# Optimization experiments

Hardware: AMD Instinct MI355X
Metric: run time of the kernel (lower is better)

## Reference

```python
import jax, jax.numpy as jnp
import numpy as np

DECAY = 0.99
EPS = 1e-05
N, K, D = 32768, 8192, 64


def setup_inputs() -> dict:
    key = jax.random.key(0)
    k1, k2, k3 = jax.random.split(key, 3)
    return {
        "inputs": jax.random.normal(k1, (N, D), dtype=jnp.float32),
        "embedding_w": jax.random.normal(k2, (K, D), dtype=jnp.float32),
        "ema_w": jax.random.normal(k3, (K, D), dtype=jnp.float32),
        "ema_cluster_size": jnp.zeros((K,), dtype=jnp.float32),
    }


def reference(inputs, embedding_w, ema_w, ema_cluster_size):
    k = embedding_w.shape[0]
    # pairwise squared L2 distances: [N, K]
    distances = (
        jnp.sum(inputs ** 2, axis=1, keepdims=True)
        + jnp.sum(embedding_w ** 2, axis=1)
        - 2.0 * inputs @ embedding_w.T
    )
    encoding_indices = jnp.argmin(distances, axis=1)           # [N] int
    encodings = jax.nn.one_hot(encoding_indices, k, dtype=inputs.dtype)  # [N, K]
    codebook = embedding_w  # returned codebook is the PRE-update weight (as in torch source)

    # EMA updates (training branch), expressed functionally
    cluster_size = ema_cluster_size * DECAY + (1.0 - DECAY) * jnp.sum(encodings, axis=0)
    n = jnp.sum(cluster_size)
    cluster_size = (cluster_size + EPS) / (n + k * EPS) * n
    dw = encodings.T @ inputs                                   # [K, D]
    ema_w_new = ema_w * DECAY + (1.0 - DECAY) * dw
    embedding_new = ema_w_new / cluster_size[:, None]

    return (encodings, codebook, cluster_size, ema_w_new, embedding_new)
```

## Files before the change

kernel.cpp:

```cpp
#include <hip/hip_runtime.h>
#include <hip/hip_bf16.h>

#define N_PTS 32768
#define K_CLU 8192
#define D_DIM 64
#define DECAYF 0.99f
#define OMDF   0.01f
#define EPSF   1e-5f

typedef _Float16 v8h __attribute__((ext_vector_type(8)));
typedef float    v4f __attribute__((ext_vector_type(4)));

#define AS1 __attribute__((address_space(1)))
#define AS3 __attribute__((address_space(3)))

#define OFF_COUNTS 0
#define OFF_DW     (32768)
#define OFF_NSUM   (OFF_DW + 2097152)
#define OFF_EHI    (OFF_NSUM + 16)
#define OFF_ELO    (OFF_EHI + 1048576)
#define OFF_E2     (OFF_ELO + 1048576)

__global__ __launch_bounds__(256) void vq_prep(
    const float* __restrict__ emb, const float* __restrict__ ema_cs,
    _Float16* __restrict__ ehi, _Float16* __restrict__ elo,
    float* __restrict__ e2, float* __restrict__ nsum)
{
    const int wave = threadIdx.x >> 6;
    const int lane = threadIdx.x & 63;
    if (blockIdx.x < 2048) {
        const int row = blockIdx.x * 4 + wave;
        float v = emb[(size_t)row * D_DIM + lane];
        _Float16 h = (_Float16)v;
        _Float16 l = (_Float16)(v - (float)h);
        const int sw = (lane & 7) | ((((lane >> 3) ^ (row & 7)) & 7) << 3);
        ehi[(size_t)row * D_DIM + sw] = h;
        elo[(size_t)row * D_DIM + sw] = l;
        float s = v * v;
        #pragma unroll
        for (int m = 1; m < 64; m <<= 1) s += __shfl_xor(s, m, 64);
        if (lane == 0) e2[row] = s;
    } else {
        const int t = (blockIdx.x - 2048) * 256 + threadIdx.x;
        float v = ema_cs[t];
        #pragma unroll
        for (int m = 1; m < 64; m <<= 1) v += __shfl_xor(v, m, 64);
        if (lane == 0) atomicAdd(nsum, v);
    }
}

__global__ __launch_bounds__(256) void vq_fused(
    const float* __restrict__ x,
    const _Float16* __restrict__ ehi, const _Float16* __restrict__ elo,
    const float* __restrict__ e2,
    float* __restrict__ enc,
    unsigned int* __restrict__ counts,
    float* __restrict__ dw)
{
    __shared__ _Float16 sEhi[2][128 * 64];
    __shared__ _Float16 sElo[2][128 * 64];
    __shared__ float    sE2[2][128];

    const int bid  = blockIdx.x;
    const int tid  = threadIdx.x;
    const int wave = tid >> 6;
    const int lane = tid & 63;
    const int quad = lane >> 4;
    const int l15  = lane & 15;
    const int ptbase = bid * 64 + wave * 16;

    v8h xh[2], xl[2];
    {
        const int pt = ptbase + l15;
        const float* xp = x + (size_t)pt * D_DIM + quad * 8;
        #pragma unroll
        for (int c = 0; c < 2; ++c) {
            float4 a = *(const float4*)(xp + c * 32);
            float4 b = *(const float4*)(xp + c * 32 + 4);
            float vv[8] = {a.x, a.y, a.z, a.w, b.x, b.y, b.z, b.w};
            v8h hh, ll;
            #pragma unroll
            for (int j = 0; j < 8; ++j) {
                _Float16 h = (_Float16)vv[j];
                hh[j] = h;
                ll[j] = (_Float16)(vv[j] - (float)h);
            }
            xh[c] = hh; xl[c] = ll;
        }
    }

    float best[4]; int bidx4[4];
    #pragma unroll
    for (int i = 0; i < 4; ++i) { best[i] = 3.4e38f; bidx4[i] = 0; }

    v4f* enc4 = (v4f*)enc;
    const size_t zbase = (size_t)bid * 131072 + tid;
    const v4f zz = {0.f, 0.f, 0.f, 0.f};

    auto stage = [&](int b, int chunk) {
        const size_t gb = (size_t)chunk * 128 * 128;
        const char* gh = (const char*)ehi + gb;
        const char* gl = (const char*)elo + gb;
        char* lh = (char*)&sEhi[b][0];
        char* ll = (char*)&sElo[b][0];
        #pragma unroll
        for (int i = 0; i < 4; ++i) {
            const int off = wave * 4096 + i * 1024;
            __builtin_amdgcn_global_load_lds(
                (const AS1 void*)(gh + off + lane * 16), (AS3 void*)(lh + off), 16, 0, 0);
            __builtin_amdgcn_global_load_lds(
                (const AS1 void*)(gl + off + lane * 16), (AS3 void*)(ll + off), 16, 0, 0);
        }
        if (wave == 0) {
            const char* ge = (const char*)(e2 + (size_t)chunk * 128);
            char* le = (char*)&sE2[b][0];
            #pragma unroll
            for (int i = 0; i < 2; ++i) {
                __builtin_amdgcn_global_load_lds(
                    (const AS1 void*)(ge + i * 256 + lane * 4), (AS3 void*)(le + i * 256), 4, 0, 0);
            }
        }
    };

    stage(0, 0);
    asm volatile("s_waitcnt vmcnt(0)" ::: "memory");
    __builtin_amdgcn_s_barrier();
    __builtin_amdgcn_sched_barrier(0);

    for (int chunk = 0; chunk < 64; ++chunk) {
        const int cur = chunk & 1;
        if (chunk + 1 < 64) stage(cur ^ 1, chunk + 1);
        __builtin_amdgcn_sched_barrier(0);

        const int kbase = chunk * 128;
        const size_t zo = zbase + (size_t)chunk * 2048;
        #pragma unroll
        for (int sub = 0; sub < 8; ++sub) {
            __builtin_nontemporal_store(zz, enc4 + zo + sub * 256);

            const int nl = sub * 16 + l15;
            const int ro = nl * 64;
            const int swz = (nl & 7) << 3;
            v8h bh0 = *(const v8h*)&sEhi[cur][ro + ((quad << 3) ^ swz)];
            v8h bh1 = *(const v8h*)&sEhi[cur][ro + (((4 + quad) << 3) ^ swz)];
            v8h bl0 = *(const v8h*)&sElo[cur][ro + ((quad << 3) ^ swz)];
            v8h bl1 = *(const v8h*)&sElo[cur][ro + (((4 + quad) << 3) ^ swz)];
            const float e2v = sE2[cur][nl];
            const int kidx = kbase + nl;
            v4f acc0 = {0.f, 0.f, 0.f, 0.f};
            v4f acc1 = {0.f, 0.f, 0.f, 0.f};
            acc0 = __builtin_amdgcn_mfma_f32_16x16x32_f16(xh[0], bh0, acc0, 0, 0, 0);
            acc1 = __builtin_amdgcn_mfma_f32_16x16x32_f16(xh[1], bh1, acc1, 0, 0, 0);
            acc0 = __builtin_amdgcn_mfma_f32_16x16x32_f16(xl[0], bh0, acc0, 0, 0, 0);
            acc1 = __builtin_amdgcn_mfma_f32_16x16x32_f16(xl[1], bh1, acc1, 0, 0, 0);
            acc0 = __builtin_amdgcn_mfma_f32_16x16x32_f16(xh[0], bl0, acc0, 0, 0, 0);
            acc1 = __builtin_amdgcn_mfma_f32_16x16x32_f16(xh[1], bl1, acc1, 0, 0, 0);
            #pragma unroll
            for (int r = 0; r < 4; ++r) {
                float dot = acc0[r] + acc1[r];
                float dist = fmaf(dot, -2.0f, e2v);
                if (dist < best[r]) { best[r] = dist; bidx4[r] = kidx; }
            }
        }

        asm volatile("s_waitcnt vmcnt(8)" ::: "memory");
        __builtin_amdgcn_s_barrier();
        __builtin_amdgcn_sched_barrier(0);
    }

    #pragma unroll
    for (int i = 0; i < 4; ++i) {
        #pragma unroll
        for (int m = 1; m < 16; m <<= 1) {
            float ov = __shfl_xor(best[i], m, 64);
            int   oi = __shfl_xor(bidx4[i], m, 64);
            if (ov < best[i] || (ov == best[i] && oi < bidx4[i])) { best[i] = ov; bidx4[i] = oi; }
        }
    }

    asm volatile("s_waitcnt vmcnt(0)" ::: "memory");
    __builtin_amdgcn_s_barrier();
    __builtin_amdgcn_sched_barrier(0);

    if (l15 == 0) {
        #pragma unroll
        for (int r = 0; r < 4; ++r) {
            int p = ptbase + quad * 4 + r;
            enc[(size_t)p * K_CLU + bidx4[r]] = 1.0f;
            atomicAdd(&counts[bidx4[r]], 1u);
        }
    }

    #pragma unroll
    for (int j = 0; j < 16; ++j) {
        const int src = (j >> 2) * 16;
        const int r = j & 3;
        int k = __shfl(bidx4[r], src, 64);
        float val = x[(size_t)(ptbase + j) * D_DIM + lane];
        atomicAdd(&dw[(size_t)k * D_DIM + lane], val);
    }
}

__global__ __launch_bounds__(256) void vq_finalize(
    const float* __restrict__ emb, const float* __restrict__ ema_w,
    const float* __restrict__ ema_cs,
    const unsigned int* __restrict__ counts, const float* __restrict__ dw,
    const float* __restrict__ nsum,
    float* __restrict__ out)
{
    const size_t ENC = (size_t)N_PTS * K_CLU;
    float* out_codebook = out + ENC;
    float* out_cs       = out_codebook + (size_t)K_CLU * D_DIM;
    float* out_ema      = out_cs + K_CLU;
    float* out_emb      = out_ema + (size_t)K_CLU * D_DIM;

    const int gid = blockIdx.x * 256 + threadIdx.x;
    const int k = gid >> 6, d = gid & 63;
    float dwv = dw[gid];
    float en  = DECAYF * ema_w[gid] + OMDF * dwv;
    float cnt = (float)counts[k];
    float cs_raw = DECAYF * ema_cs[k] + OMDF * cnt;
    float n  = DECAYF * nsum[0] + OMDF * (float)N_PTS;
    float cs = (cs_raw + EPSF) / (n + (float)K_CLU * EPSF) * n;
    out_codebook[gid] = emb[gid];
    out_ema[gid] = en;
    out_emb[gid] = en / cs;
    if (d == 0) out_cs[k] = cs;
}

extern "C" void kernel_launch(void* const* d_in, const int* in_sizes, int n_in,
                              void* d_out, int out_size, void* d_ws, size_t ws_size,
                              hipStream_t stream)
{
    const float* x      = (const float*)d_in[0];
    const float* emb    = (const float*)d_in[1];
    const float* ema_w  = (const float*)d_in[2];
    const float* ema_cs = (const float*)d_in[3];
    float* out = (float*)d_out;
    char* ws = (char*)d_ws;

    unsigned int* counts = (unsigned int*)(ws + OFF_COUNTS);
    float*        dw     = (float*)(ws + OFF_DW);
    float*        nsum   = (float*)(ws + OFF_NSUM);
    _Float16*     ehi    = (_Float16*)(ws + OFF_EHI);
    _Float16*     elo    = (_Float16*)(ws + OFF_ELO);
    float*        e2     = (float*)(ws + OFF_E2);

    hipMemsetAsync(ws + OFF_COUNTS, 0, (OFF_NSUM + 16) - OFF_COUNTS, stream);

    vq_prep<<<2080, 256, 0, stream>>>(emb, ema_cs, ehi, elo, e2, nsum);
    vq_fused<<<512, 256, 0, stream>>>(x, ehi, elo, e2, out, counts, dw);
    vq_finalize<<<2048, 256, 0, stream>>>(emb, ema_w, ema_cs, counts, dw, nsum, out);
}
```

Baseline: 1.069 ms.

## Split one-hot encoding write out of argmin kernel into separate pass

```diff
diff --git a/kernel.cpp b/kernel.cpp
--- a/kernel.cpp
+++ b/kernel.cpp
@@ -49,7 +49,7 @@
     }
 }
 
-__global__ __launch_bounds__(256) void vq_fused(
+__global__ __launch_bounds__(256) void vq_argmin(
     const float* __restrict__ x,
     const _Float16* __restrict__ ehi, const _Float16* __restrict__ elo,
     const float* __restrict__ e2,
@@ -93,10 +93,6 @@
     #pragma unroll
     for (int i = 0; i < 4; ++i) { best[i] = 3.4e38f; bidx4[i] = 0; }
 
-    v4f* enc4 = (v4f*)enc;
-    const size_t zbase = (size_t)bid * 131072 + tid;
-    const v4f zz = {0.f, 0.f, 0.f, 0.f};
-
     auto stage = [&](int b, int chunk) {
         const size_t gb = (size_t)chunk * 128 * 128;
         const char* gh = (const char*)ehi + gb;
@@ -133,11 +129,8 @@
         __builtin_amdgcn_sched_barrier(0);
 
         const int kbase = chunk * 128;
-        const size_t zo = zbase + (size_t)chunk * 2048;
         #pragma unroll
         for (int sub = 0; sub < 8; ++sub) {
-            __builtin_nontemporal_store(zz, enc4 + zo + sub * 256);
-
             const int nl = sub * 16 + l15;
             const int ro = nl * 64;
             const int swz = (nl & 7) << 3;
@@ -163,7 +156,7 @@
             }
         }
 
-        asm volatile("s_waitcnt vmcnt(8)" ::: "memory");
+        asm volatile("s_waitcnt vmcnt(0)" ::: "memory");
         __builtin_amdgcn_s_barrier();
         __builtin_amdgcn_sched_barrier(0);
     }
@@ -178,15 +171,11 @@
         }
     }
 
-    asm volatile("s_waitcnt vmcnt(0)" ::: "memory");
-    __builtin_amdgcn_s_barrier();
-    __builtin_amdgcn_sched_barrier(0);
-
     if (l15 == 0) {
         #pragma unroll
         for (int r = 0; r < 4; ++r) {
             int p = ptbase + quad * 4 + r;
-            enc[(size_t)p * K_CLU + bidx4[r]] = 1.0f;
+            *(unsigned int*)(enc + (size_t)p * K_CLU) = (unsigned int)bidx4[r];
             atomicAdd(&counts[bidx4[r]], 1u);
         }
     }
@@ -198,6 +187,31 @@
         int k = __shfl(bidx4[r], src, 64);
         float val = x[(size_t)(ptbase + j) * D_DIM + lane];
         atomicAdd(&dw[(size_t)k * D_DIM + lane], val);
+    }
+}
+
+__global__ __launch_bounds__(256) void vq_encwrite(float* __restrict__ enc)
+{
+    const int tid = threadIdx.x;
+    unsigned int ki[4];
+    #pragma unroll
+    for (int ri = 0; ri < 4; ++ri) {
+        const int row = blockIdx.x * 4 + ri;
+        ki[ri] = *(const unsigned int*)(enc + (size_t)row * K_CLU);
+    }
+    __syncthreads();
+    #pragma unroll
+    for (int ri = 0; ri < 4; ++ri) {
+        const int row = blockIdx.x * 4 + ri;
+        float* rp = enc + (size_t)row * K_CLU + tid * 32;
+        const int fbase = tid * 32;
+        #pragma unroll
+        for (int j = 0; j < 8; ++j) {
+            v4f v = {0.f, 0.f, 0.f, 0.f};
+            const int d = (int)ki[ri] - (fbase + j * 4);
+            if (d >= 0 && d < 4) v[d] = 1.0f;
+            *(v4f*)(rp + j * 4) = v;
+        }
     }
 }
 
@@ -249,6 +263,7 @@
     hipMemsetAsync(ws + OFF_COUNTS, 0, (OFF_NSUM + 16) - OFF_COUNTS, stream);
 
     vq_prep<<<2080, 256, 0, stream>>>(emb, ema_cs, ehi, elo, e2, nsum);
-    vq_fused<<<512, 256, 0, stream>>>(x, ehi, elo, e2, out, counts, dw);
+    vq_argmin<<<512, 256, 0, stream>>>(x, ehi, elo, e2, out, counts, dw);
+    vq_encwrite<<<8192, 256, 0, stream>>>(out);
     vq_finalize<<<2048, 256, 0, stream>>>(emb, ema_w, ema_cs, counts, dw, nsum, out);
 }
```

Result: slower. 1.339 ms (+25.3%).
